# Kernel tuning notes

Hardware: AMD Instinct MI355X
Metric: run time of the kernel (lower is better)

Reference implementation:

```python
import jax, jax.numpy as jnp
import numpy as np

HEAD_DIM = 64
FEAT_H, FEAT_W = 64, 64
ROPE_THETA = 10000.0


def axial_rope_cache(dim, height, width, theta):
    # Matches compute_axial_rope_cache: interleaved cos/sin of shape [H*W, dim]
    theta_dim = (dim // 2) // 2
    freqs = 1.0 / theta ** (jnp.arange(theta_dim, dtype=jnp.float32) * 2.0 / theta_dim)
    t_x = jnp.tile(jnp.arange(width, dtype=jnp.float32)[None, :], (height, 1)).reshape(-1)
    t_y = jnp.tile(jnp.arange(height, dtype=jnp.float32)[:, None], (1, width)).reshape(-1)
    theta_all = jnp.concatenate([jnp.outer(t_x, freqs), jnp.outer(t_y, freqs)], axis=-1)
    cos = jnp.repeat(jnp.cos(theta_all), 2, axis=-1)  # [H*W, dim]
    sin = jnp.repeat(jnp.sin(theta_all), 2, axis=-1)
    return cos, sin


def apply_rope(x, cos, sin):
    # x: [B, H, N, D]; cos/sin: [N, D]
    x1 = x[..., 0::2]
    x2 = x[..., 1::2]
    rot = jnp.stack([-x2, x1], axis=-1).reshape(x.shape)
    return x * cos[None, None] + rot * sin[None, None]


def setup_inputs() -> dict:
    key = jax.random.key(0)
    ks = jax.random.split(key, 11)
    B, Nq, Nk, E, KVD, ID = 1, 4096, 8192, 256, 64, 256
    s_e = 1.0 / np.sqrt(E)
    s_kv = 1.0 / np.sqrt(KVD)
    s_i = 1.0 / np.sqrt(ID)
    return {
        "query": jax.random.normal(ks[0], (B, Nq, E), jnp.float32),
        "key": jax.random.normal(ks[1], (B, Nk, KVD), jnp.float32),
        "value": jax.random.normal(ks[2], (B, Nk, KVD), jnp.float32),
        "Wq": jax.random.normal(ks[3], (E, ID), jnp.float32) * s_e,
        "bq": jnp.zeros((ID,), jnp.float32),
        "Wk": jax.random.normal(ks[4], (KVD, ID), jnp.float32) * s_kv,
        "bk": jnp.zeros((ID,), jnp.float32),
        "Wv": jax.random.normal(ks[5], (KVD, ID), jnp.float32) * s_kv,
        "bv": jnp.zeros((ID,), jnp.float32),
        "Wo": jax.random.normal(ks[6], (ID, E), jnp.float32) * s_i,
        "bo": jnp.zeros((E,), jnp.float32),
        "num_k_exclude_rope": 0,
    }


def reference(query, key, value, Wq, bq, Wk, bk, Wv, bv, Wo, bo, num_k_exclude_rope):
    B, Nq, _ = query.shape
    Nk = key.shape[1]
    H, D = 4, HEAD_DIM

    def split_heads(x):
        b, n, c = x.shape
        return x.reshape(b, n, H, c // H).transpose(0, 2, 1, 3)

    q = split_heads(query @ Wq + bq)  # [B,H,Nq,D]
    k = split_heads(key @ Wk + bk)    # [B,H,Nk,D]
    v = split_heads(value @ Wv + bv)

    cos, sin = axial_rope_cache(D, FEAT_H, FEAT_W, ROPE_THETA)  # [4096, D]
    q = apply_rope(q, cos, sin)

    num_k_rope = Nk - num_k_exclude_rope
    k_spatial = k[:, :, :num_k_rope, :]
    k_other = k[:, :, num_k_rope:, :]
    repeats = num_k_rope // cos.shape[0]  # rope_k_repeat=True
    cos_k = jnp.tile(cos, (repeats, 1))
    sin_k = jnp.tile(sin, (repeats, 1))
    k_spatial = apply_rope(k_spatial, cos_k, sin_k)
    k = jnp.concatenate([k_spatial, k_other], axis=2)

    q = q / jnp.sqrt(jnp.asarray(D, q.dtype))
    scores = jnp.einsum("bhqd,bhkd->bhqk", q, k)
    attn = jax.nn.softmax(scores, axis=-1)
    out = jnp.einsum("bhqk,bhkd->bhqd", attn, v)
    out = out.transpose(0, 2, 1, 3).reshape(B, Nq, H * D)
    return out @ Wo + bo
```

## Files before the change

### kernel.cpp

```cpp
#include <hip/hip_runtime.h>
#include <hip/hip_bf16.h>

#define H 4
#define NQ 4096
#define NK 8192
#define D 64
#define BK 64
#define NSPLIT 8
#define KSPAN (NK / NSPLIT)
#define PST 72

#define QSCALE 0.1803368801111204f

typedef short v8s __attribute__((ext_vector_type(8)));
typedef float v4f __attribute__((ext_vector_type(4)));

static __device__ __forceinline__ unsigned short f2bf(float f) {
    unsigned int u = __float_as_uint(f);
    u = (u + 0x7FFFu + ((u >> 16) & 1u)) >> 16;
    return (unsigned short)u;
}
static __device__ __forceinline__ float bf2f(unsigned short h) {
    return __uint_as_float(((unsigned int)h) << 16);
}
static __device__ __forceinline__ unsigned int pkbf(float a, float b) {
    union { __hip_bfloat162 h; unsigned int u; } cv;
    cv.h = __float22bfloat162_rn(make_float2(a, b));
    return cv.u;
}
static __device__ __forceinline__ void split8(const float* a, v8s& hi, v8s& lo) {
#pragma unroll
    for (int j = 0; j < 8; ++j) {
        unsigned short h = f2bf(a[j]);
        hi[j] = (short)h;
        lo[j] = (short)f2bf(a[j] - bf2f(h));
    }
}
static __device__ __forceinline__ void dma16(const unsigned short* g, unsigned short* l) {
    __builtin_amdgcn_global_load_lds(
        (const __attribute__((address_space(1))) unsigned int*)(const void*)g,
        (__attribute__((address_space(3))) unsigned int*)(void*)l, 16, 0, 0);
}

__global__ __launch_bounds__(256) void wprep_kernel(
    const float* __restrict__ Wq, const float* __restrict__ Wk,
    const float* __restrict__ Wv, const float* __restrict__ Wo,
    unsigned short* __restrict__ Wqt, unsigned short* __restrict__ Wkt,
    unsigned short* __restrict__ Wvt, unsigned short* __restrict__ Wot)
{
    int i = blockIdx.x * 256 + threadIdx.x;
    const float* src; unsigned short* dst; int idx, sh;
    if (i < 65536)       { src = Wq; dst = Wqt; idx = i;          sh = 8; }
    else if (i < 81920)  { src = Wk; dst = Wkt; idx = i - 65536;  sh = 6; }
    else if (i < 98304)  { src = Wv; dst = Wvt; idx = i - 81920;  sh = 6; }
    else                 { src = Wo; dst = Wot; idx = i - 98304;  sh = 8; }
    const int K = 1 << sh;
    const int c = idx >> sh, e = idx & (K - 1);
    const float v = src[e * 256 + c];
    const unsigned short h = f2bf(v);
    dst[idx] = h;
    dst[idx + (K << 8)] = f2bf(v - bf2f(h));
}

__global__ __launch_bounds__(256) void qkv_kernel(
    const float* __restrict__ query, const float* __restrict__ key,
    const float* __restrict__ value,
    const unsigned short* __restrict__ Wqt, const unsigned short* __restrict__ Wkt,
    const unsigned short* __restrict__ Wvt,
    const float* __restrict__ bq, const float* __restrict__ bk,
    const float* __restrict__ bv,
    unsigned short* __restrict__ Qb, unsigned short* __restrict__ Kb,
    unsigned short* __restrict__ Vt, const int* __restrict__ nexp)
{
    const int b = blockIdx.x;
    const int t = threadIdx.x, w = t >> 6, lane = t & 63;
    const int quad = lane >> 4, l16 = lane & 15;
    const int colbase = w * 64;

    if (b < 128) {
        const int n0 = b * 32;
        v4f acc[2][4];
#pragma unroll
        for (int st = 0; st < 2; ++st)
#pragma unroll
            for (int ct = 0; ct < 4; ++ct) {
                const float bb = bq[colbase + ct * 16 + l16];
                acc[st][ct] = v4f{bb, bb, bb, bb};
            }
#pragma unroll
        for (int k0 = 0; k0 < 256; k0 += 32) {
            v8s ah[2], al[2];
#pragma unroll
            for (int st = 0; st < 2; ++st) {
                float av[8];
                const float* ar = query + (size_t)(n0 + st * 16 + l16) * 256 + k0 + quad * 8;
                *(float4*)av = *(const float4*)ar;
                *(float4*)(av + 4) = *(const float4*)(ar + 4);
                split8(av, ah[st], al[st]);
            }
#pragma unroll
            for (int ct = 0; ct < 4; ++ct) {
                const unsigned short* wp = Wqt + (size_t)(colbase + ct * 16 + l16) * 256 + k0 + quad * 8;
                const v8s wh = *(const v8s*)wp;
                const v8s wl = *(const v8s*)(wp + 65536);
#pragma unroll
                for (int st = 0; st < 2; ++st) {
                    acc[st][ct] = __builtin_amdgcn_mfma_f32_16x16x32_bf16(al[st], wh, acc[st][ct], 0, 0, 0);
                    acc[st][ct] = __builtin_amdgcn_mfma_f32_16x16x32_bf16(ah[st], wl, acc[st][ct], 0, 0, 0);
                    acc[st][ct] = __builtin_amdgcn_mfma_f32_16x16x32_bf16(ah[st], wh, acc[st][ct], 0, 0, 0);
                }
            }
        }
#pragma unroll
        for (int ct = 0; ct < 4; ++ct) {
            const int d = ct * 16 + l16;
            const int j = d >> 1;
            const float freq = exp2f(-(float)(j & 15) * 1.66096404744368f);
            const bool isx = (j < 16), odd = (d & 1);
#pragma unroll
            for (int st = 0; st < 2; ++st)
#pragma unroll
                for (int r = 0; r < 4; ++r) {
                    const int p = n0 + st * 16 + quad * 4 + r;
                    const float tpos = isx ? (float)(p & 63) : (float)(p >> 6);
                    float sn, cs;
                    __sincosf(tpos * freq, &sn, &cs);
                    const float x = acc[st][ct][r];
                    const float xp = __shfl_xor(x, 1, 64);
                    const float y = odd ? fmaf(x, cs, xp * sn) : fmaf(x, cs, -xp * sn);
                    Qb[((size_t)(w * NQ + p) << 6) + d] = f2bf(y * QSCALE);
                }
        }
    } else {
        const bool isK = (b < 384);
        const int n0 = (isK ? (b - 128) : (b - 384)) * 32;
        const float* X = isK ? key : value;
        const unsigned short* Wt = isK ? Wkt : Wvt;
        const float* bias = isK ? bk : bv;
        v8s wf[4][2][2];
#pragma unroll
        for (int ct = 0; ct < 4; ++ct)
#pragma unroll
            for (int k = 0; k < 2; ++k) {
                const unsigned short* wp = Wt + (size_t)(colbase + ct * 16 + l16) * 64 + k * 32 + quad * 8;
                wf[ct][k][0] = *(const v8s*)wp;
                wf[ct][k][1] = *(const v8s*)(wp + 16384);
            }
        v4f acc[2][4];
#pragma unroll
        for (int st = 0; st < 2; ++st)
#pragma unroll
            for (int ct = 0; ct < 4; ++ct) {
                const float bb = bias[colbase + ct * 16 + l16];
                acc[st][ct] = v4f{bb, bb, bb, bb};
            }
#pragma unroll
        for (int st = 0; st < 2; ++st)
#pragma unroll
            for (int k = 0; k < 2; ++k) {
                float av[8];
                const float* ar = X + (size_t)(n0 + st * 16 + l16) * 64 + k * 32 + quad * 8;
                *(float4*)av = *(const float4*)ar;
                *(float4*)(av + 4) = *(const float4*)(ar + 4);
                v8s ah, al;
                split8(av, ah, al);
#pragma unroll
                for (int ct = 0; ct < 4; ++ct) {
                    acc[st][ct] = __builtin_amdgcn_mfma_f32_16x16x32_bf16(al, wf[ct][k][0], acc[st][ct], 0, 0, 0);
                    acc[st][ct] = __builtin_amdgcn_mfma_f32_16x16x32_bf16(ah, wf[ct][k][1], acc[st][ct], 0, 0, 0);
                    acc[st][ct] = __builtin_amdgcn_mfma_f32_16x16x32_bf16(ah, wf[ct][k][0], acc[st][ct], 0, 0, 0);
                }
            }
        if (isK) {
            const int nro = NK - *nexp;
#pragma unroll
            for (int ct = 0; ct < 4; ++ct) {
                const int d = ct * 16 + l16;
                const int j = d >> 1;
                const float freq = exp2f(-(float)(j & 15) * 1.66096404744368f);
                const bool isx = (j < 16), odd = (d & 1);
#pragma unroll
                for (int st = 0; st < 2; ++st)
#pragma unroll
                    for (int r = 0; r < 4; ++r) {
                        const int p = n0 + st * 16 + quad * 4 + r;
                        const int pc = p & 4095;
                        const float tpos = isx ? (float)(pc & 63) : (float)(pc >> 6);
                        float sn, cs;
                        __sincosf(tpos * freq, &sn, &cs);
                        const float x = acc[st][ct][r];
                        const float xp = __shfl_xor(x, 1, 64);
                        float y = odd ? fmaf(x, cs, xp * sn) : fmaf(x, cs, -xp * sn);
                        y = (p < nro) ? y : x;
                        Kb[((size_t)(w * NK + p) << 6) + d] = f2bf(y);
                    }
            }
        } else {
#pragma unroll
            for (int ct = 0; ct < 4; ++ct) {
                const int col = colbase + ct * 16 + l16;
#pragma unroll
                for (int st = 0; st < 2; ++st) {
                    uint2 u = make_uint2(pkbf(acc[st][ct][0], acc[st][ct][1]),
                                         pkbf(acc[st][ct][2], acc[st][ct][3]));
                    *(uint2*)(Vt + (size_t)col * NK + n0 + st * 16 + quad * 4) = u;
                }
            }
        }
    }
}

__global__ __launch_bounds__(256) void attn_kernel(
    const unsigned short* __restrict__ Qb, const unsigned short* __restrict__ Kb,
    const unsigned short* __restrict__ Vt, unsigned short* __restrict__ Opart,
    float* __restrict__ Lbuf)
{
    __shared__ alignas(16) unsigned short Kl[64 * 64];
    __shared__ alignas(16) unsigned short Vl[64 * 64];
    __shared__ alignas(16) unsigned short Pl[4 * 32 * PST];

    const int blk = blockIdx.x;
    const int s = blk & 7, h = (blk >> 3) & 3, qt = blk >> 5;
    const int t = threadIdx.x;
    const int w = t >> 6, lane = t & 63;
    const int quad = lane >> 4, l16 = lane & 15;

    const int q0 = qt * 128 + w * 32;
    v8s qf[2][2];
#pragma unroll
    for (int g = 0; g < 2; ++g) {
        const unsigned short* qr = Qb + ((size_t)(h * NQ + q0 + g * 16 + l16) << 6) + quad * 8;
        qf[g][0] = *(const v8s*)qr;
        qf[g][1] = *(const v8s*)(qr + 32);
    }

    v4f O[4][2];
#pragma unroll
    for (int dt = 0; dt < 4; ++dt)
#pragma unroll
        for (int g = 0; g < 2; ++g) O[dt][g] = v4f{0.f, 0.f, 0.f, 0.f};
    float psum[2] = {0.f, 0.f};

    const unsigned short* Kbase = Kb + (((size_t)h * NK + s * KSPAN) << 6);
    const unsigned short* Vbase = Vt + (size_t)(h * 64) * NK + s * KSPAN;

    const int srow = lane >> 3;
    const int schunk = (lane & 7) ^ srow;
    const int c0off = ((quad ^ (l16 & 7)) * 8);
    const int c1off = c0off ^ 32;
    unsigned short* Pw = &Pl[w * 32 * PST];

    for (int k0 = 0; k0 < KSPAN; k0 += BK) {
        __syncthreads();
#pragma unroll
        for (int half = 0; half < 2; ++half) {
            const int r0 = w * 16 + half * 8;
            dma16(Kbase + ((size_t)(k0 + r0 + srow) << 6) + schunk * 8, &Kl[r0 * 64]);
            dma16(Vbase + (size_t)(r0 + srow) * NK + k0 + schunk * 8, &Vl[r0 * 64]);
        }
        __syncthreads();

#pragma unroll
        for (int tt = 0; tt < 4; ++tt) {
            const unsigned short* kr = &Kl[(tt * 16 + l16) * 64];
            const v8s kf0 = *(const v8s*)(kr + c0off);
            const v8s kf1 = *(const v8s*)(kr + c1off);
#pragma unroll
            for (int g = 0; g < 2; ++g) {
                v4f a = v4f{0.f, 0.f, 0.f, 0.f};
                a = __builtin_amdgcn_mfma_f32_16x16x32_bf16(kf0, qf[g][0], a, 0, 0, 0);
                a = __builtin_amdgcn_mfma_f32_16x16x32_bf16(kf1, qf[g][1], a, 0, 0, 0);
                const float e0 = __builtin_amdgcn_exp2f(a[0]);
                const float e1 = __builtin_amdgcn_exp2f(a[1]);
                const float e2 = __builtin_amdgcn_exp2f(a[2]);
                const float e3 = __builtin_amdgcn_exp2f(a[3]);
                psum[g] += (e0 + e1) + (e2 + e3);
                *(uint2*)(&Pw[(g * 16 + l16) * PST + tt * 16 + quad * 4]) =
                    make_uint2(pkbf(e0, e1), pkbf(e2, e3));
            }
        }
        __asm__ volatile("s_waitcnt lgkmcnt(0)" ::: "memory");

        v8s pf[2][2];
#pragma unroll
        for (int g = 0; g < 2; ++g) {
            const unsigned short* pr = &Pw[(g * 16 + l16) * PST + quad * 8];
            pf[g][0] = *(const v8s*)pr;
            pf[g][1] = *(const v8s*)(pr + 32);
        }
#pragma unroll
        for (int dt = 0; dt < 4; ++dt) {
            const unsigned short* vr = &Vl[(dt * 16 + l16) * 64];
            const v8s vf0 = *(const v8s*)(vr + c0off);
            const v8s vf1 = *(const v8s*)(vr + c1off);
#pragma unroll
            for (int g = 0; g < 2; ++g) {
                v4f a = O[dt][g];
                a = __builtin_amdgcn_mfma_f32_16x16x32_bf16(vf0, pf[g][0], a, 0, 0, 0);
                a = __builtin_amdgcn_mfma_f32_16x16x32_bf16(vf1, pf[g][1], a, 0, 0, 0);
                O[dt][g] = a;
            }
        }
    }

#pragma unroll
    for (int g = 0; g < 2; ++g) {
        float p = psum[g];
        p += __shfl_xor(p, 16, 64);
        p += __shfl_xor(p, 32, 64);
        psum[g] = p;
    }
    unsigned short* Ob = Opart + (size_t)blk * 8192;
#pragma unroll
    for (int g = 0; g < 2; ++g) {
        const int row = w * 32 + g * 16 + l16;
#pragma unroll
        for (int dt = 0; dt < 4; ++dt) {
            uint2 u = make_uint2(pkbf(O[dt][g][0], O[dt][g][1]),
                                 pkbf(O[dt][g][2], O[dt][g][3]));
            *(uint2*)(Ob + row * 64 + dt * 16 + quad * 4) = u;
        }
        if (quad == 0) Lbuf[blk * 128 + row] = psum[g];
    }
}

__global__ __launch_bounds__(256) void oproj_kernel(
    const unsigned short* __restrict__ Opart, const float* __restrict__ Lbuf,
    const unsigned short* __restrict__ Wt, const float* __restrict__ bo,
    float* __restrict__ out)
{
    const int t = threadIdx.x, w = t >> 6, lane = t & 63;
    const int quad = lane >> 4, l16 = lane & 15;
    const int n0 = blockIdx.x * 16, colbase = w * 64;
    const int qt = n0 >> 7, rbase = n0 & 127;

    v4f facc[4];
#pragma unroll
    for (int ct = 0; ct < 4; ++ct) facc[ct] = v4f{0.f, 0.f, 0.f, 0.f};

#pragma unroll 1
    for (int hh = 0; hh < 4; ++hh) {
        v8s wfr[4][2][2];
#pragma unroll
        for (int ct = 0; ct < 4; ++ct)
#pragma unroll
            for (int ch = 0; ch < 2; ++ch) {
                const unsigned short* wp = Wt + (size_t)(colbase + ct * 16 + l16) * 256 + hh * 64 + ch * 32 + quad * 8;
                wfr[ct][ch][0] = *(const v8s*)wp;
                wfr[ct][ch][1] = *(const v8s*)(wp + 65536);
            }
        v4f hacc[4];
#pragma unroll
        for (int ct = 0; ct < 4; ++ct) hacc[ct] = v4f{0.f, 0.f, 0.f, 0.f};
        float4 lsum = make_float4(0.f, 0.f, 0.f, 0.f);
#pragma unroll
        for (int sp = 0; sp < NSPLIT; ++sp) {
            const int slab = (qt * 4 + hh) * 8 + sp;
            const unsigned short* arow = Opart + (size_t)slab * 8192 + (rbase + l16) * 64;
#pragma unroll
            for (int ch = 0; ch < 2; ++ch) {
                const v8s A = *(const v8s*)(arow + ch * 32 + quad * 8);
#pragma unroll
                for (int ct = 0; ct < 4; ++ct) {
                    hacc[ct] = __builtin_amdgcn_mfma_f32_16x16x32_bf16(A, wfr[ct][ch][0], hacc[ct], 0, 0, 0);
                    hacc[ct] = __builtin_amdgcn_mfma_f32_16x16x32_bf16(A, wfr[ct][ch][1], hacc[ct], 0, 0, 0);
                }
            }
            const float4 lv = *(const float4*)(Lbuf + slab * 128 + rbase + quad * 4);
            lsum.x += lv.x; lsum.y += lv.y; lsum.z += lv.z; lsum.w += lv.w;
        }
        const float li[4] = {1.f / lsum.x, 1.f / lsum.y, 1.f / lsum.z, 1.f / lsum.w};
#pragma unroll
        for (int ct = 0; ct < 4; ++ct)
#pragma unroll
            for (int r = 0; r < 4; ++r)
                facc[ct][r] = fmaf(hacc[ct][r], li[r], facc[ct][r]);
    }
#pragma unroll
    for (int ct = 0; ct < 4; ++ct) {
        const float bb = bo[colbase + ct * 16 + l16];
#pragma unroll
        for (int r = 0; r < 4; ++r)
            out[(size_t)(n0 + quad * 4 + r) * 256 + colbase + ct * 16 + l16] = facc[ct][r] + bb;
    }
}

extern "C" void kernel_launch(void* const* d_in, const int* in_sizes, int n_in,
                              void* d_out, int out_size, void* d_ws, size_t ws_size,
                              hipStream_t stream) {
    const float* query = (const float*)d_in[0];
    const float* key   = (const float*)d_in[1];
    const float* value = (const float*)d_in[2];
    const float* Wq    = (const float*)d_in[3];
    const float* bq    = (const float*)d_in[4];
    const float* Wk    = (const float*)d_in[5];
    const float* bk    = (const float*)d_in[6];
    const float* Wv    = (const float*)d_in[7];
    const float* bv    = (const float*)d_in[8];
    const float* Wo    = (const float*)d_in[9];
    const float* bo    = (const float*)d_in[10];
    const int*   nex   = (const int*)d_in[11];

    char* ws = (char*)d_ws;
    unsigned short* Qb  = (unsigned short*)(ws);
    unsigned short* Kb  = (unsigned short*)(ws + (size_t)2  * 1024 * 1024);
    unsigned short* Vt  = (unsigned short*)(ws + (size_t)6  * 1024 * 1024);
    unsigned short* Opart = (unsigned short*)(ws + (size_t)10 * 1024 * 1024);
    float* Lbuf         = (float*)(ws + (size_t)26 * 1024 * 1024);
    char* wbase         = ws + (size_t)26 * 1024 * 1024 + 512 * 1024;
    unsigned short* Wqt = (unsigned short*)(wbase);
    unsigned short* Wkt = (unsigned short*)(wbase + 256 * 1024);
    unsigned short* Wvt = (unsigned short*)(wbase + 320 * 1024);
    unsigned short* Wot = (unsigned short*)(wbase + 384 * 1024);
    float* out          = (float*)d_out;

    wprep_kernel<<<640, 256, 0, stream>>>(Wq, Wk, Wv, Wo, Wqt, Wkt, Wvt, Wot);
    qkv_kernel<<<640, 256, 0, stream>>>(query, key, value, Wqt, Wkt, Wvt,
                                        bq, bk, bv, Qb, Kb, Vt, nex);
    attn_kernel<<<1024, 256, 0, stream>>>(Qb, Kb, Vt, Opart, Lbuf);
    oproj_kernel<<<256, 256, 0, stream>>>(Opart, Lbuf, Wot, bo, out);
}
```

Before: 180.2 us.

## Drop weight-prep kernel and reduce split-K attention partials via float atomics

Removes the separate weight transpose/split kernel: projections now gather fp32 weights with strided loads and split them to hi/lo bf16 in-register. The attention kernel no longer writes per-split bf16 partial outputs and row sums. It atomically adds fp32 partials into a single accumulator that is zeroed by a memset, so the output projection reads one normalized slab instead of eight. This cuts a kernel launch and the partial-buffer traffic, but adds atomic contention, a memset, and uncoalesced strided weight reads repeated in every block. The output projection also moves from two MFMA passes on pre-split weights to three MFMA passes with a split activation.

```diff
diff --git a/kernel.cpp b/kernel.cpp
--- a/kernel.cpp
+++ b/kernel.cpp
@@ -1,13 +1,11 @@
 #include <hip/hip_runtime.h>
 #include <hip/hip_bf16.h>
 
-#define H 4
 #define NQ 4096
 #define NK 8192
-#define D 64
-#define BK 64
 #define NSPLIT 8
 #define KSPAN (NK / NSPLIT)
+#define BK 64
 #define PST 72
 
 #define QSCALE 0.1803368801111204f
@@ -36,37 +34,24 @@
         lo[j] = (short)f2bf(a[j] - bf2f(h));
     }
 }
+static __device__ __forceinline__ void wgather(const float* __restrict__ W,
+                                               int k0, int col, v8s& wh, v8s& wl) {
+    float wv[8];
+#pragma unroll
+    for (int j = 0; j < 8; ++j) wv[j] = W[(size_t)(k0 + j) * 256 + col];
+    split8(wv, wh, wl);
+}
 static __device__ __forceinline__ void dma16(const unsigned short* g, unsigned short* l) {
     __builtin_amdgcn_global_load_lds(
         (const __attribute__((address_space(1))) unsigned int*)(const void*)g,
         (__attribute__((address_space(3))) unsigned int*)(void*)l, 16, 0, 0);
 }
 
-__global__ __launch_bounds__(256) void wprep_kernel(
-    const float* __restrict__ Wq, const float* __restrict__ Wk,
-    const float* __restrict__ Wv, const float* __restrict__ Wo,
-    unsigned short* __restrict__ Wqt, unsigned short* __restrict__ Wkt,
-    unsigned short* __restrict__ Wvt, unsigned short* __restrict__ Wot)
-{
-    int i = blockIdx.x * 256 + threadIdx.x;
-    const float* src; unsigned short* dst; int idx, sh;
-    if (i < 65536)       { src = Wq; dst = Wqt; idx = i;          sh = 8; }
-    else if (i < 81920)  { src = Wk; dst = Wkt; idx = i - 65536;  sh = 6; }
-    else if (i < 98304)  { src = Wv; dst = Wvt; idx = i - 81920;  sh = 6; }
-    else                 { src = Wo; dst = Wot; idx = i - 98304;  sh = 8; }
-    const int K = 1 << sh;
-    const int c = idx >> sh, e = idx & (K - 1);
-    const float v = src[e * 256 + c];
-    const unsigned short h = f2bf(v);
-    dst[idx] = h;
-    dst[idx + (K << 8)] = f2bf(v - bf2f(h));
-}
-
 __global__ __launch_bounds__(256) void qkv_kernel(
     const float* __restrict__ query, const float* __restrict__ key,
     const float* __restrict__ value,
-    const unsigned short* __restrict__ Wqt, const unsigned short* __restrict__ Wkt,
-    const unsigned short* __restrict__ Wvt,
+    const float* __restrict__ Wq, const float* __restrict__ Wk,
+    const float* __restrict__ Wv,
     const float* __restrict__ bq, const float* __restrict__ bk,
     const float* __restrict__ bv,
     unsigned short* __restrict__ Qb, unsigned short* __restrict__ Kb,
@@ -100,9 +85,8 @@
             }
 #pragma unroll
             for (int ct = 0; ct < 4; ++ct) {
-                const unsigned short* wp = Wqt + (size_t)(colbase + ct * 16 + l16) * 256 + k0 + quad * 8;
-                const v8s wh = *(const v8s*)wp;
-                const v8s wl = *(const v8s*)(wp + 65536);
+                v8s wh, wl;
+                wgather(Wq, k0 + quad * 8, colbase + ct * 16 + l16, wh, wl);
 #pragma unroll
                 for (int st = 0; st < 2; ++st) {
                     acc[st][ct] = __builtin_amdgcn_mfma_f32_16x16x32_bf16(al[st], wh, acc[st][ct], 0, 0, 0);
@@ -135,17 +119,8 @@
         const bool isK = (b < 384);
         const int n0 = (isK ? (b - 128) : (b - 384)) * 32;
         const float* X = isK ? key : value;
-        const unsigned short* Wt = isK ? Wkt : Wvt;
+        const float* W = isK ? Wk : Wv;
         const float* bias = isK ? bk : bv;
-        v8s wf[4][2][2];
-#pragma unroll
-        for (int ct = 0; ct < 4; ++ct)
-#pragma unroll
-            for (int k = 0; k < 2; ++k) {
-                const unsigned short* wp = Wt + (size_t)(colbase + ct * 16 + l16) * 64 + k * 32 + quad * 8;
-                wf[ct][k][0] = *(const v8s*)wp;
-                wf[ct][k][1] = *(const v8s*)(wp + 16384);
-            }
         v4f acc[2][4];
 #pragma unroll
         for (int st = 0; st < 2; ++st)
@@ -155,22 +130,28 @@
                 acc[st][ct] = v4f{bb, bb, bb, bb};
             }
 #pragma unroll
-        for (int st = 0; st < 2; ++st)
-#pragma unroll
-            for (int k = 0; k < 2; ++k) {
+        for (int k0 = 0; k0 < 64; k0 += 32) {
+            v8s ah[2], al[2];
+#pragma unroll
+            for (int st = 0; st < 2; ++st) {
                 float av[8];
-                const float* ar = X + (size_t)(n0 + st * 16 + l16) * 64 + k * 32 + quad * 8;
+                const float* ar = X + (size_t)(n0 + st * 16 + l16) * 64 + k0 + quad * 8;
                 *(float4*)av = *(const float4*)ar;
                 *(float4*)(av + 4) = *(const float4*)(ar + 4);
-                v8s ah, al;
-                split8(av, ah, al);
-#pragma unroll
-                for (int ct = 0; ct < 4; ++ct) {
-                    acc[st][ct] = __builtin_amdgcn_mfma_f32_16x16x32_bf16(al, wf[ct][k][0], acc[st][ct], 0, 0, 0);
-                    acc[st][ct] = __builtin_amdgcn_mfma_f32_16x16x32_bf16(ah, wf[ct][k][1], acc[st][ct], 0, 0, 0);
-                    acc[st][ct] = __builtin_amdgcn_mfma_f32_16x16x32_bf16(ah, wf[ct][k][0], acc[st][ct], 0, 0, 0);
+                split8(av, ah[st], al[st]);
+            }
+#pragma unroll
+            for (int ct = 0; ct < 4; ++ct) {
+                v8s wh, wl;
+                wgather(W, k0 + quad * 8, colbase + ct * 16 + l16, wh, wl);
+#pragma unroll
+                for (int st = 0; st < 2; ++st) {
+                    acc[st][ct] = __builtin_amdgcn_mfma_f32_16x16x32_bf16(al[st], wh, acc[st][ct], 0, 0, 0);
+                    acc[st][ct] = __builtin_amdgcn_mfma_f32_16x16x32_bf16(ah[st], wl, acc[st][ct], 0, 0, 0);
+                    acc[st][ct] = __builtin_amdgcn_mfma_f32_16x16x32_bf16(ah[st], wh, acc[st][ct], 0, 0, 0);
                 }
             }
+        }
         if (isK) {
             const int nro = NK - *nexp;
 #pragma unroll
@@ -212,8 +193,8 @@
 
 __global__ __launch_bounds__(256) void attn_kernel(
     const unsigned short* __restrict__ Qb, const unsigned short* __restrict__ Kb,
-    const unsigned short* __restrict__ Vt, unsigned short* __restrict__ Opart,
-    float* __restrict__ Lbuf)
+    const unsigned short* __restrict__ Vt, float* __restrict__ Osum,
+    float* __restrict__ Lsum)
 {
     __shared__ alignas(16) unsigned short Kl[64 * 64];
     __shared__ alignas(16) unsigned short Vl[64 * 64];
@@ -305,84 +286,66 @@
 
 #pragma unroll
     for (int g = 0; g < 2; ++g) {
+        const int q = q0 + g * 16 + l16;
+        float* orow = Osum + ((size_t)(h * NQ + q) << 6);
+#pragma unroll
+        for (int dt = 0; dt < 4; ++dt)
+#pragma unroll
+            for (int r = 0; r < 4; ++r)
+                unsafeAtomicAdd(orow + dt * 16 + quad * 4 + r, O[dt][g][r]);
         float p = psum[g];
         p += __shfl_xor(p, 16, 64);
         p += __shfl_xor(p, 32, 64);
-        psum[g] = p;
-    }
-    unsigned short* Ob = Opart + (size_t)blk * 8192;
-#pragma unroll
-    for (int g = 0; g < 2; ++g) {
-        const int row = w * 32 + g * 16 + l16;
-#pragma unroll
-        for (int dt = 0; dt < 4; ++dt) {
-            uint2 u = make_uint2(pkbf(O[dt][g][0], O[dt][g][1]),
-                                 pkbf(O[dt][g][2], O[dt][g][3]));
-            *(uint2*)(Ob + row * 64 + dt * 16 + quad * 4) = u;
-        }
-        if (quad == 0) Lbuf[blk * 128 + row] = psum[g];
+        if (quad == 0) unsafeAtomicAdd(Lsum + h * NQ + q, p);
     }
 }
 
 __global__ __launch_bounds__(256) void oproj_kernel(
-    const unsigned short* __restrict__ Opart, const float* __restrict__ Lbuf,
-    const unsigned short* __restrict__ Wt, const float* __restrict__ bo,
+    const float* __restrict__ Osum, const float* __restrict__ Lsum,
+    const float* __restrict__ Wo, const float* __restrict__ bo,
     float* __restrict__ out)
 {
     const int t = threadIdx.x, w = t >> 6, lane = t & 63;
     const int quad = lane >> 4, l16 = lane & 15;
     const int n0 = blockIdx.x * 16, colbase = w * 64;
-    const int qt = n0 >> 7, rbase = n0 & 127;
-
-    v4f facc[4];
-#pragma unroll
-    for (int ct = 0; ct < 4; ++ct) facc[ct] = v4f{0.f, 0.f, 0.f, 0.f};
-
-#pragma unroll 1
-    for (int hh = 0; hh < 4; ++hh) {
-        v8s wfr[4][2][2];
-#pragma unroll
-        for (int ct = 0; ct < 4; ++ct)
-#pragma unroll
-            for (int ch = 0; ch < 2; ++ch) {
-                const unsigned short* wp = Wt + (size_t)(colbase + ct * 16 + l16) * 256 + hh * 64 + ch * 32 + quad * 8;
-                wfr[ct][ch][0] = *(const v8s*)wp;
-                wfr[ct][ch][1] = *(const v8s*)(wp + 65536);
-            }
-        v4f hacc[4];
-#pragma unroll
-        for (int ct = 0; ct < 4; ++ct) hacc[ct] = v4f{0.f, 0.f, 0.f, 0.f};
-        float4 lsum = make_float4(0.f, 0.f, 0.f, 0.f);
-#pragma unroll
-        for (int sp = 0; sp < NSPLIT; ++sp) {
-            const int slab = (qt * 4 + hh) * 8 + sp;
-            const unsigned short* arow = Opart + (size_t)slab * 8192 + (rbase + l16) * 64;
-#pragma unroll
-            for (int ch = 0; ch < 2; ++ch) {
-                const v8s A = *(const v8s*)(arow + ch * 32 + quad * 8);
-#pragma unroll
-                for (int ct = 0; ct < 4; ++ct) {
-                    hacc[ct] = __builtin_amdgcn_mfma_f32_16x16x32_bf16(A, wfr[ct][ch][0], hacc[ct], 0, 0, 0);
-                    hacc[ct] = __builtin_amdgcn_mfma_f32_16x16x32_bf16(A, wfr[ct][ch][1], hacc[ct], 0, 0, 0);
-                }
-            }
-            const float4 lv = *(const float4*)(Lbuf + slab * 128 + rbase + quad * 4);
-            lsum.x += lv.x; lsum.y += lv.y; lsum.z += lv.z; lsum.w += lv.w;
-        }
-        const float li[4] = {1.f / lsum.x, 1.f / lsum.y, 1.f / lsum.z, 1.f / lsum.w};
-#pragma unroll
-        for (int ct = 0; ct < 4; ++ct)
-#pragma unroll
-            for (int r = 0; r < 4; ++r)
-                facc[ct][r] = fmaf(hacc[ct][r], li[r], facc[ct][r]);
-    }
+    const int n = n0 + l16;
+
+    float linv[4];
+#pragma unroll
+    for (int hh = 0; hh < 4; ++hh) linv[hh] = 1.f / Lsum[hh * NQ + n];
+
+    v4f acc[4];
 #pragma unroll
     for (int ct = 0; ct < 4; ++ct) {
         const float bb = bo[colbase + ct * 16 + l16];
+        acc[ct] = v4f{bb, bb, bb, bb};
+    }
+#pragma unroll
+    for (int k0 = 0; k0 < 256; k0 += 32) {
+        const int hh = k0 >> 6;
+        const int d0 = (k0 & 63) + quad * 8;
+        float av[8];
+        const float* ar = Osum + ((size_t)(hh * NQ + n) << 6) + d0;
+        *(float4*)av = *(const float4*)ar;
+        *(float4*)(av + 4) = *(const float4*)(ar + 4);
+#pragma unroll
+        for (int j = 0; j < 8; ++j) av[j] *= linv[hh];
+        v8s ah, al;
+        split8(av, ah, al);
+#pragma unroll
+        for (int ct = 0; ct < 4; ++ct) {
+            v8s wh, wl;
+            wgather(Wo, k0 + quad * 8, colbase + ct * 16 + l16, wh, wl);
+            acc[ct] = __builtin_amdgcn_mfma_f32_16x16x32_bf16(al, wh, acc[ct], 0, 0, 0);
+            acc[ct] = __builtin_amdgcn_mfma_f32_16x16x32_bf16(ah, wl, acc[ct], 0, 0, 0);
+            acc[ct] = __builtin_amdgcn_mfma_f32_16x16x32_bf16(ah, wh, acc[ct], 0, 0, 0);
+        }
+    }
+#pragma unroll
+    for (int ct = 0; ct < 4; ++ct)
 #pragma unroll
         for (int r = 0; r < 4; ++r)
-            out[(size_t)(n0 + quad * 4 + r) * 256 + colbase + ct * 16 + l16] = facc[ct][r] + bb;
-    }
+            out[(size_t)(n0 + quad * 4 + r) * 256 + colbase + ct * 16 + l16] = acc[ct][r];
 }
 
 extern "C" void kernel_launch(void* const* d_in, const int* in_sizes, int n_in,
@@ -402,21 +365,16 @@
     const int*   nex   = (const int*)d_in[11];
 
     char* ws = (char*)d_ws;
-    unsigned short* Qb  = (unsigned short*)(ws);
-    unsigned short* Kb  = (unsigned short*)(ws + (size_t)2  * 1024 * 1024);
-    unsigned short* Vt  = (unsigned short*)(ws + (size_t)6  * 1024 * 1024);
-    unsigned short* Opart = (unsigned short*)(ws + (size_t)10 * 1024 * 1024);
-    float* Lbuf         = (float*)(ws + (size_t)26 * 1024 * 1024);
-    char* wbase         = ws + (size_t)26 * 1024 * 1024 + 512 * 1024;
-    unsigned short* Wqt = (unsigned short*)(wbase);
-    unsigned short* Wkt = (unsigned short*)(wbase + 256 * 1024);
-    unsigned short* Wvt = (unsigned short*)(wbase + 320 * 1024);
-    unsigned short* Wot = (unsigned short*)(wbase + 384 * 1024);
-    float* out          = (float*)d_out;
-
-    wprep_kernel<<<640, 256, 0, stream>>>(Wq, Wk, Wv, Wo, Wqt, Wkt, Wvt, Wot);
-    qkv_kernel<<<640, 256, 0, stream>>>(query, key, value, Wqt, Wkt, Wvt,
+    unsigned short* Qb = (unsigned short*)(ws);
+    unsigned short* Kb = (unsigned short*)(ws + (size_t)2 * 1024 * 1024);
+    unsigned short* Vt = (unsigned short*)(ws + (size_t)6 * 1024 * 1024);
+    float* Osum        = (float*)(ws + (size_t)10 * 1024 * 1024);
+    float* Lsum        = (float*)(ws + (size_t)14 * 1024 * 1024);
+    float* out         = (float*)d_out;
+
+    hipMemsetAsync(Osum, 0, (size_t)4 * 1024 * 1024 + 64 * 1024, stream);
+    qkv_kernel<<<640, 256, 0, stream>>>(query, key, value, Wq, Wk, Wv,
                                         bq, bk, bv, Qb, Kb, Vt, nex);
-    attn_kernel<<<1024, 256, 0, stream>>>(Qb, Kb, Vt, Opart, Lbuf);
-    oproj_kernel<<<256, 256, 0, stream>>>(Opart, Lbuf, Wot, bo, out);
-}
+    attn_kernel<<<1024, 256, 0, stream>>>(Qb, Kb, Vt, Osum, Lsum);
+    oproj_kernel<<<256, 256, 0, stream>>>(Osum, Lsum, Wo, bo, out);
+}
```

New measurement: 241.3 us. 1.34x slower.
